# Performance work log

Measured on AMD Instinct MI355X. Metric: run time of the kernel, lower is better.

## Reference

```python
import jax, jax.numpy as jnp
import numpy as np

B, T, D = 1, 2048, 4096
N, K, H = 32, 8, 128  # num_heads, num_kv_heads, head_dim
ROPE_BASE = 10000
SCALE_FACTOR = 1.0
EPS = 1e-6
NEG_INF = -1e9


def rms_norm(x):
    var = jnp.mean(jnp.square(x), axis=-1, keepdims=True)
    return x * jax.lax.rsqrt(var + EPS)


def apply_rope(x, positions, base_frequency, scale_factor=1.0):
    # x: [B, L, num_heads, H], positions: [B, L]
    head_dim = x.shape[-1]
    fraction = 2.0 * jnp.arange(head_dim // 2, dtype=jnp.float32) / head_dim
    timescale = base_frequency ** fraction  # [H/2]
    sinusoid = positions[..., None].astype(jnp.float32) / timescale  # [B,L,H/2]
    sinusoid = sinusoid[..., None, :] / scale_factor  # [B,L,1,H/2]
    sin, cos = jnp.sin(sinusoid), jnp.cos(sinusoid)
    x1, x2 = jnp.split(x, 2, axis=-1)
    return jnp.concatenate([x1 * cos - x2 * sin, x2 * cos + x1 * sin], axis=-1)


def setup_inputs() -> dict:
    key = jax.random.key(0)
    ks = jax.random.split(key, 7)
    x = jax.random.normal(ks[0], (B, T, D), dtype=jnp.float32)
    segment_pos = jnp.broadcast_to(jnp.arange(T, dtype=jnp.int32)[None, :], (B, T))
    causal = jnp.tril(jnp.ones((T, T), dtype=bool))
    attn_mask = jnp.where(causal, 0.0, NEG_INF).astype(jnp.float32)[None]  # [B,T,S]
    attn_mask = jnp.broadcast_to(attn_mask, (B, T, T))
    q_w = jax.random.normal(ks[1], (N, D, H), dtype=jnp.float32) * (D ** -0.5)
    kv_w = jax.random.normal(ks[2], (2, K, D, H), dtype=jnp.float32) * (D ** -0.5)
    o_w = jax.random.normal(ks[3], (N, H, D), dtype=jnp.float32) * ((N * H) ** -0.5)
    q_scale = jax.random.normal(ks[4], (H,), dtype=jnp.float32) * 0.02  # RMSNorm scale (zeros-init style)
    k_scale = jax.random.normal(ks[5], (H,), dtype=jnp.float32) * 0.02
    return {"x": x, "segment_pos": segment_pos, "attn_mask": attn_mask,
            "q_w": q_w, "kv_w": kv_w, "o_w": o_w,
            "q_scale": q_scale, "k_scale": k_scale}


def reference(x, segment_pos, attn_mask, q_w, kv_w, o_w, q_scale, k_scale):
    # Projections
    q = jnp.einsum('BTD,NDH->BTNH', x, q_w)          # [B,T,N,H]
    kv = jnp.einsum('BSD,CKDH->CBSKH', x, kv_w)      # [2,B,S,K,H]
    k, v = kv[0], kv[1]
    # QK RMSNorm (with scale, (1+scale) convention) and value RMSNorm (no scale)
    q = rms_norm(q) * (1.0 + q_scale)
    k = rms_norm(k) * (1.0 + k_scale)
    v = rms_norm(v)
    # RoPE (standard path: positions are [B,L])
    q = apply_rope(q, segment_pos, ROPE_BASE, SCALE_FACTOR)
    k = apply_rope(k, segment_pos, ROPE_BASE, SCALE_FACTOR)
    # GQA grouping: [B,T,K,G,H]
    G = N // K
    qg = q.reshape(B, T, K, G, H)
    attn_logits = jnp.einsum('btkgh,bskh->bkgts', qg, k)  # [B,K,G,T,S]
    attn_logits = attn_logits + attn_mask[:, None, None, :, :]
    attn_weights = jax.nn.softmax(attn_logits, axis=-1).astype(v.dtype)
    out = jnp.einsum('bkgts,bskh->btkgh', attn_weights, v)  # [B,T,K,G,H]
    out = out.reshape(B, T, N, H)
    return jnp.einsum('BTNH,NHD->BTD', out, o_w)
```

## Files before the change

### kernel.cpp

```cpp
#include <hip/hip_runtime.h>
#include <stdint.h>


typedef __bf16 bf16x8 __attribute__((ext_vector_type(8)));
typedef float  f32x4  __attribute__((ext_vector_type(4)));

__device__ __forceinline__ uint16_t f2bf(float f) {
    union { float f; uint32_t u; } v; v.f = f;
    uint32_t r = v.u + 0x7fffu + ((v.u >> 16) & 1u);
    return (uint16_t)(r >> 16);
}

__device__ __forceinline__ void gload_lds16(const void* g, void* l) {
    __builtin_amdgcn_global_load_lds(
        (const __attribute__((address_space(1))) uint32_t*)g,
        (__attribute__((address_space(3))) uint32_t*)l, 16, 0, 0);
}

__global__ __launch_bounds__(256) void k_cvt_x(const float* __restrict__ x,
                                               uint16_t* __restrict__ xb) {
    int i = (blockIdx.x * 256 + threadIdx.x) * 8;
    int r = i >> 12, k = i & 4095;
    float4 a = *(const float4*)(x + i);
    float4 b = *(const float4*)(x + i + 4);
    uint16_t tmp[8];
    tmp[0] = f2bf(a.x); tmp[1] = f2bf(a.y); tmp[2] = f2bf(a.z); tmp[3] = f2bf(a.w);
    tmp[4] = f2bf(b.x); tmp[5] = f2bf(b.y); tmp[6] = f2bf(b.z); tmp[7] = f2bf(b.w);
    int dst = r * 4096 + (k & ~63) + (((((k >> 3) & 7) ^ (r & 7))) << 3);
    *(uint4*)(xb + dst) = *(uint4*)tmp;
}

__global__ __launch_bounds__(256) void k_prep_wt(const float* __restrict__ qw,
                                                 const float* __restrict__ kvw,
                                                 uint16_t* __restrict__ Wt) {
    const int hx = blockIdx.x, dx = blockIdx.y, m = blockIdx.z;
    const float* src = (m < 32) ? (qw + (size_t)m * 524288)
                                : (kvw + (size_t)(m - 32) * 524288);
    __shared__ uint16_t tile[64][65];
    const int t = threadIdx.x, d0 = dx * 64, h0 = hx * 64;
#pragma unroll
    for (int i = 0; i < 16; ++i) {
        int idx = i * 256 + t, r = idx >> 6, c = idx & 63;
        tile[r][c] = f2bf(src[(size_t)(d0 + r) * 128 + h0 + c]);
    }
    __syncthreads();
#pragma unroll
    for (int it = 0; it < 2; ++it) {
        int slot = it * 256 + t, hr = slot >> 3, cl = slot & 7;
        int R = m * 128 + h0 + hr;
        uint16_t tmp[8];
#pragma unroll
        for (int e = 0; e < 8; ++e) tmp[e] = tile[cl * 8 + e][hr];
        *(uint4*)&Wt[(size_t)R * 4096 + d0 + ((cl ^ (R & 7)) << 3)] = *(uint4*)tmp;
    }
}

__global__ __launch_bounds__(256) void k_prep_ot(const float* __restrict__ ow,
                                                 uint16_t* __restrict__ Ot) {
    const int dx = blockIdx.x, hx = blockIdx.y, n = blockIdx.z;
    const float* src = ow + (size_t)n * 524288;
    __shared__ uint16_t tile[64][65];
    const int t = threadIdx.x, h0 = hx * 64, d0 = dx * 64;
#pragma unroll
    for (int i = 0; i < 16; ++i) {
        int idx = i * 256 + t, r = idx >> 6, c = idx & 63;
        tile[r][c] = f2bf(src[(size_t)(h0 + r) * 4096 + d0 + c]);
    }
    __syncthreads();
#pragma unroll
    for (int it = 0; it < 2; ++it) {
        int slot = it * 256 + t, dr = slot >> 3, cl = slot & 7;
        int R = d0 + dr;
        uint16_t tmp[8];
#pragma unroll
        for (int e = 0; e < 8; ++e) tmp[e] = tile[cl * 8 + e][dr];
        *(uint4*)&Ot[(size_t)R * 4096 + n * 128 + h0 + ((cl ^ (R & 7)) << 3)] = *(uint4*)tmp;
    }
}

#define PH_BAR do { asm volatile("" ::: "memory"); \
                    __builtin_amdgcn_s_barrier(); \
                    asm volatile("" ::: "memory"); } while (0)
#define WAIT_VM(N) do { asm volatile("s_waitcnt vmcnt(" #N ")" ::: "memory"); \
                        __builtin_amdgcn_sched_barrier(0); } while (0)
#define SCHED0 __builtin_amdgcn_sched_barrier(0)

__global__ __launch_bounds__(512, 2) void k_gemm_qkv(const uint16_t* __restrict__ A,
                                                     const uint16_t* __restrict__ Bt,
                                                     const int* __restrict__ pos,
                                                     const float* __restrict__ qs,
                                                     const float* __restrict__ ks,
                                                     uint16_t* __restrict__ Qg,
                                                     uint16_t* __restrict__ Kg,
                                                     uint16_t* __restrict__ Vg) {
    extern __shared__ __align__(16) char smem[];
    uint16_t* lds = (uint16_t*)smem;
    const int Kd = 4096;
    const int t = threadIdx.x, wid = t >> 6, lane = t & 63;
    const int l16 = lane & 15, quad = lane >> 4;
    const int wr = wid >> 2, wc = wid & 3;
    const int bx = blockIdx.x, bm0 = blockIdx.y * 256, bn0 = bx * 256;

    f32x4 acc[8][4];
    const f32x4 z4 = {0.f, 0.f, 0.f, 0.f};
#pragma unroll
    for (int i = 0; i < 8; ++i)
#pragma unroll
        for (int j = 0; j < 4; ++j) acc[i][j] = z4;

    const int r0 = wid * 16 + (lane >> 2), c4 = lane & 3;
    const int sw2 = (r0 >> 1) & 3, sw7 = r0 & 7;
    const int offK0 = (((c4 ^ sw2)) ^ sw7) * 8;
    const int offK1 = ((4 + (c4 ^ sw2)) ^ sw7) * 8;
    const uint16_t* pA0 = A + (size_t)(bm0 + r0) * Kd;
    const uint16_t* pA1 = pA0 + (size_t)128 * Kd;
    const uint16_t* pB0 = Bt + (size_t)(bn0 + r0) * Kd;
    const uint16_t* pB1 = pB0 + (size_t)128 * Kd;
    uint16_t* stA = lds + wid * 512;
    uint16_t* stB = lds + 32768 + wid * 512;

    const int sA = (l16 >> 1) & 3;
    const int rdA = (wr * 128 + l16) * 32 + ((quad ^ sA) << 3);
    const int rdB = 32768 + (wc * 64 + l16) * 32 + ((quad ^ sA) << 3);

    bf16x8 afA[4], afB[4], bfA[4], bfB[4];

#define STAGE_A(SLAB, OFF, TT) do { \
    gload_lds16(pA0 + (size_t)(TT) * 64 + (OFF), stA + (SLAB) * 8192); \
    gload_lds16(pA1 + (size_t)(TT) * 64 + (OFF), stA + (SLAB) * 8192 + 4096); } while (0)
#define STAGE_B(SLAB, OFF, TT) do { \
    gload_lds16(pB0 + (size_t)(TT) * 64 + (OFF), stB + (SLAB) * 8192); \
    gload_lds16(pB1 + (size_t)(TT) * 64 + (OFF), stB + (SLAB) * 8192 + 4096); } while (0)
#define RD_A(DST, SLAB, I0) do { _Pragma("unroll") \
    for (int i_ = 0; i_ < 4; ++i_) \
        DST[i_] = *(const bf16x8*)&lds[(SLAB) * 8192 + rdA + ((I0) + i_) * 512]; } while (0)
#define RD_B(DST, SLAB) do { _Pragma("unroll") \
    for (int j_ = 0; j_ < 4; ++j_) \
        DST[j_] = *(const bf16x8*)&lds[(SLAB) * 8192 + rdB + j_ * 512]; } while (0)
#define MFMA16(AF, BF, I0) do { __builtin_amdgcn_s_setprio(1); \
    _Pragma("unroll") for (int i_ = 0; i_ < 4; ++i_) \
        _Pragma("unroll") for (int j_ = 0; j_ < 4; ++j_) \
            acc[(I0) + i_][j_] = __builtin_amdgcn_mfma_f32_16x16x32_bf16(AF[i_], BF[j_], acc[(I0) + i_][j_], 0, 0, 0); \
    __builtin_amdgcn_s_setprio(0); } while (0)

#define TILE(TT, BUF) do { \
    RD_A(afB, 2*(BUF), 4); \
    WAIT_VM(4); \
    STAGE_A(2*((BUF)^1)+1, offK1, (TT)+1); \
    SCHED0; MFMA16(afA, bfA, 0); PH_BAR; \
    RD_A(afA, 2*(BUF)+1, 0); RD_B(bfB, 2*(BUF)+1); \
    STAGE_B(2*((BUF)^1)+1, offK1, (TT)+1); \
    SCHED0; MFMA16(afB, bfA, 4); PH_BAR; \
    RD_A(afB, 2*(BUF)+1, 4); \
    WAIT_VM(4); \
    STAGE_A(2*(BUF), offK0, (TT)+2); \
    SCHED0; MFMA16(afA, bfB, 0); PH_BAR; \
    RD_A(afA, 2*((BUF)^1), 0); RD_B(bfA, 2*((BUF)^1)); \
    STAGE_B(2*(BUF), offK0, (TT)+2); \
    SCHED0; MFMA16(afB, bfB, 4); PH_BAR; \
} while (0)

    STAGE_A(0, offK0, 0); STAGE_B(0, offK0, 0);
    STAGE_A(1, offK1, 0); STAGE_B(1, offK1, 0);
    STAGE_A(2, offK0, 1); STAGE_B(2, offK0, 1);
    WAIT_VM(8);
    PH_BAR;
    RD_A(afA, 0, 0); RD_B(bfA, 0);

#pragma unroll 1
    for (int Ti = 0; Ti < 31; ++Ti) {
        TILE(2 * Ti, 0);
        TILE(2 * Ti + 1, 1);
    }

    RD_A(afB, 0, 4); WAIT_VM(4); STAGE_A(3, offK1, 63);
    SCHED0; MFMA16(afA, bfA, 0); PH_BAR;
    RD_A(afA, 1, 0); RD_B(bfB, 1); STAGE_B(3, offK1, 63);
    SCHED0; MFMA16(afB, bfA, 4); PH_BAR;
    RD_A(afB, 1, 4); WAIT_VM(4);
    SCHED0; MFMA16(afA, bfB, 0); PH_BAR;
    RD_A(afA, 2, 0); RD_B(bfA, 2);
    SCHED0; MFMA16(afB, bfB, 4); PH_BAR;
    RD_A(afB, 2, 4); WAIT_VM(0);
    SCHED0; MFMA16(afA, bfA, 0); PH_BAR;
    RD_A(afA, 3, 0); RD_B(bfB, 3);
    SCHED0; MFMA16(afB, bfA, 4); PH_BAR;
    RD_A(afB, 3, 4);
    SCHED0; MFMA16(afA, bfB, 0); PH_BAR;
    SCHED0; MFMA16(afB, bfB, 4);

#undef TILE
#undef MFMA16
#undef RD_B
#undef RD_A
#undef STAGE_B
#undef STAGE_A

    float* X   = (float*)smem;
    float* ssq = (float*)(smem + 133120);

#pragma unroll
    for (int i = 0; i < 8; ++i)
#pragma unroll
        for (int r = 0; r < 4; ++r) {
            float s = 0.f;
#pragma unroll
            for (int j = 0; j < 4; ++j) s += acc[i][j][r] * acc[i][j][r];
            s += __shfl_xor(s, 1); s += __shfl_xor(s, 2);
            s += __shfl_xor(s, 4); s += __shfl_xor(s, 8);
            if (l16 == 0)
                ssq[(wr * 128 + i * 16 + quad * 4 + r) * 4 + (wc >> 1) * 2 + (wc & 1)] = s;
        }
    __syncthreads();

    const int cat = (bx < 16) ? 0 : (bx < 20 ? 1 : 2);
    float s1 = 0.f, s2 = 0.f, invts = 0.f;
    if (cat < 2) {
        const float* sc = cat ? ks : qs;
        s1 = 1.0f + sc[lane];
        s2 = 1.0f + sc[lane + 64];
        invts = exp2f((float)lane * -0.20762050593046014f);
    }

#pragma unroll
    for (int pass = 0; pass < 2; ++pass) {
        if (wr == pass) {
#pragma unroll
            for (int i = 0; i < 8; ++i)
#pragma unroll
                for (int j = 0; j < 4; ++j)
#pragma unroll
                    for (int r = 0; r < 4; ++r)
                        X[(i * 16 + quad * 4 + r) * 260 + wc * 64 + j * 16 + l16] = acc[i][j][r];
        }
        __syncthreads();
        for (int rr = 0; rr < 16; ++rr) {
            const int lrow = wid * 16 + rr;
            const int grow = bm0 + pass * 128 + lrow;
            float sn = 0.f, cs = 0.f;
            if (cat < 2) {
                float ang = (float)pos[grow] * invts;
                __sincosf(ang, &sn, &cs);
            }
#pragma unroll
            for (int hh = 0; hh < 2; ++hh) {
                const int sb = (pass * 128 + lrow) * 4 + hh * 2;
                float rn = rsqrtf((ssq[sb] + ssq[sb + 1]) * 0.0078125f + 1e-6f);
                float x1 = X[lrow * 260 + hh * 128 + lane];
                float x2 = X[lrow * 260 + hh * 128 + 64 + lane];
                if (cat < 2) {
                    float y1 = x1 * rn * s1, y2 = x2 * rn * s2;
                    X[lrow * 260 + hh * 128 + lane]      = y1 * cs - y2 * sn;
                    X[lrow * 260 + hh * 128 + 64 + lane] = y2 * cs + y1 * sn;
                } else {
                    X[lrow * 260 + hh * 128 + lane]      = x1 * rn;
                    X[lrow * 260 + hh * 128 + 64 + lane] = x2 * rn;
                }
            }
        }
        __syncthreads();
        if (cat == 2) {
#pragma unroll
            for (int it = 0; it < 8; ++it) {
                int slot = it * 512 + t, hh = slot >> 11, rem = slot & 2047;
                int h = rem >> 4, sc2 = rem & 15;
                uint16_t tmp[8];
#pragma unroll
                for (int e = 0; e < 8; ++e)
                    tmp[e] = f2bf(X[(sc2 * 8 + e) * 260 + hh * 128 + h]);
                int n = bx * 2 + hh;
                *(uint4*)&Vg[((size_t)(n - 40) * 128 + h) * 2048 + (bm0 + pass * 128)
                             + ((sc2 ^ (h & 15)) << 3)] = *(uint4*)tmp;
            }
        } else {
#pragma unroll
            for (int it = 0; it < 8; ++it) {
                int slot = it * 512 + t, hh = slot >> 11, rem = slot & 2047;
                int lrow = rem >> 4, c = rem & 15;
                int tg = bm0 + pass * 128 + lrow, n = bx * 2 + hh;
                f32x4 a = *(f32x4*)&X[lrow * 260 + hh * 128 + c * 8];
                f32x4 b = *(f32x4*)&X[lrow * 260 + hh * 128 + c * 8 + 4];
                uint16_t tmp[8];
#pragma unroll
                for (int e = 0; e < 4; ++e) { tmp[e] = f2bf(a[e]); tmp[4 + e] = f2bf(b[e]); }
                if (cat == 0)
                    *(uint4*)&Qg[((size_t)n * 2048 + tg) * 128 + c * 8] = *(uint4*)tmp;
                else
                    *(uint4*)&Kg[((size_t)(n - 32) * 2048 + tg) * 128
                                 + ((c ^ (tg & 15)) << 3)] = *(uint4*)tmp;
            }
        }
        __syncthreads();
    }
}

__global__ __launch_bounds__(512, 2) void k_gemm2p(const uint16_t* __restrict__ A,
                                                   const uint16_t* __restrict__ Bt,
                                                   float* __restrict__ C) {
    extern __shared__ __align__(16) char smem2[];
    uint16_t* lds = (uint16_t*)smem2;
    const int Kd = 4096, Nn = 4096;
    const int t = threadIdx.x, wid = t >> 6, lane = t & 63;
    const int l16 = lane & 15, quad = lane >> 4;
    const int wr = wid >> 1, wc = wid & 1;
    const int bm0 = blockIdx.y * 256, bn0 = blockIdx.x * 128;

    f32x4 acc[4][4];
    const f32x4 z4 = {0.f, 0.f, 0.f, 0.f};
#pragma unroll
    for (int i = 0; i < 4; ++i)
#pragma unroll
        for (int j = 0; j < 4; ++j) acc[i][j] = z4;

    const int r0 = wid * 16 + (lane >> 2), c4 = lane & 3;
    const int sw2 = (r0 >> 1) & 3, sw7 = r0 & 7;
    const int offK0 = ((c4 ^ sw2) ^ sw7) * 8;
    const int offK1 = ((4 + (c4 ^ sw2)) ^ sw7) * 8;
    const uint16_t* pA0 = A + (size_t)(bm0 + r0) * Kd;
    const uint16_t* pA1 = pA0 + (size_t)128 * Kd;
    const uint16_t* pB0 = Bt + (size_t)(bn0 + r0) * Kd;
    uint16_t* stA = lds + wid * 512;
    uint16_t* stB = lds + 49152 + wid * 512;

    const int sA = (l16 >> 1) & 3;
    const int rdA = (wr * 64 + l16) * 32 + ((quad ^ sA) << 3);
    const int rdB = 49152 + (wc * 64 + l16) * 32 + ((quad ^ sA) << 3);

    bf16x8 afA[4], afB[4], bfA[4], bfB[4];

#define G2_STAGE(SLAB, OFF, TT) do { \
    gload_lds16(pA0 + (size_t)(TT) * 64 + (OFF), stA + (SLAB) * 8192); \
    gload_lds16(pA1 + (size_t)(TT) * 64 + (OFF), stA + (SLAB) * 8192 + 4096); \
    gload_lds16(pB0 + (size_t)(TT) * 64 + (OFF), stB + (SLAB) * 4096); } while (0)
#define G2_RD(AD, BD, CS) do { _Pragma("unroll") \
    for (int i_ = 0; i_ < 4; ++i_) \
        AD[i_] = *(const bf16x8*)&lds[(CS) * 8192 + rdA + i_ * 512]; \
    _Pragma("unroll") for (int j_ = 0; j_ < 4; ++j_) \
        BD[j_] = *(const bf16x8*)&lds[(CS) * 4096 + rdB + j_ * 512]; } while (0)
#define G2_MFMA(AF, BF) do { __builtin_amdgcn_s_setprio(1); \
    _Pragma("unroll") for (int i_ = 0; i_ < 4; ++i_) \
        _Pragma("unroll") for (int j_ = 0; j_ < 4; ++j_) \
            acc[i_][j_] = __builtin_amdgcn_mfma_f32_16x16x32_bf16(AF[i_], BF[j_], acc[i_][j_], 0, 0, 0); \
    __builtin_amdgcn_s_setprio(0); } while (0)

#define G2_PH(RA, RB, CSN, SST, OFF, TT, MA, MB) do { \
    G2_RD(RA, RB, CSN); \
    WAIT_VM(3); \
    G2_STAGE(SST, OFF, TT); \
    SCHED0; G2_MFMA(MA, MB); PH_BAR; } while (0)

    G2_STAGE(0, offK0, 0);
    G2_STAGE(1, offK1, 0);
    G2_STAGE(2, offK0, 1);
    G2_STAGE(3, offK1, 1);
    WAIT_VM(6);
    PH_BAR;
    G2_RD(afA, bfA, 0);

#pragma unroll 1
    for (int m = 0; m < 20; ++m) {
        G2_PH(afB, bfB, 1, 4, offK0, 3*m + 2, afA, bfA);
        G2_PH(afA, bfA, 2, 5, offK1, 3*m + 2, afB, bfB);
        G2_PH(afB, bfB, 3, 0, offK0, 3*m + 3, afA, bfA);
        G2_PH(afA, bfA, 4, 1, offK1, 3*m + 3, afB, bfB);
        G2_PH(afB, bfB, 5, 2, offK0, 3*m + 4, afA, bfA);
        G2_PH(afA, bfA, 0, 3, offK1, 3*m + 4, afB, bfB);
    }
    G2_PH(afB, bfB, 1, 4, offK0, 62, afA, bfA);
    G2_PH(afA, bfA, 2, 5, offK1, 62, afB, bfB);
    G2_PH(afB, bfB, 3, 0, offK0, 63, afA, bfA);
    G2_PH(afA, bfA, 4, 1, offK1, 63, afB, bfB);
    G2_RD(afB, bfB, 5); WAIT_VM(3); SCHED0; G2_MFMA(afA, bfA); PH_BAR;
    G2_RD(afA, bfA, 0); WAIT_VM(0); SCHED0; G2_MFMA(afB, bfB); PH_BAR;
    G2_RD(afB, bfB, 1);              SCHED0; G2_MFMA(afA, bfA); PH_BAR;
    SCHED0; G2_MFMA(afB, bfB);

#undef G2_PH
#undef G2_MFMA
#undef G2_RD
#undef G2_STAGE

#pragma unroll
    for (int i = 0; i < 4; ++i)
#pragma unroll
        for (int j = 0; j < 4; ++j) {
            int row = bm0 + wr * 64 + i * 16 + quad * 4;
            int col = bn0 + wc * 64 + j * 16 + l16;
            float* cp = C + (size_t)row * Nn + col;
            cp[0]              = acc[i][j][0];
            cp[(size_t)Nn]     = acc[i][j][1];
            cp[2 * (size_t)Nn] = acc[i][j][2];
            cp[3 * (size_t)Nn] = acc[i][j][3];
        }
}

__global__ __launch_bounds__(512, 2) void k_attn(const uint16_t* __restrict__ Q,
                                                 const uint16_t* __restrict__ K,
                                                 const uint16_t* __restrict__ Vt,
                                                 uint16_t* __restrict__ att) {
    extern __shared__ __align__(16) char asmem[];
    uint16_t* sK = (uint16_t*)asmem;
    uint16_t* sV = sK + 16384;
    uint16_t* sP = sK + 32768;
    const int p = blockIdx.x, n = blockIdx.y, kk = n >> 2;
    const int t = threadIdx.x, wid = t >> 6, lane = t & 63;
    const int l16 = lane & 15, quad = lane >> 4;
    const int grp = wid >> 2, wsub = wid & 3;
    const int nk_a = p + 1, nk_b = 16 - p;
    const int nk_w = grp ? nk_b : nk_a;
    const int qbase = (grp ? (15 - p) * 128 : p * 128) + wsub * 32;
    const f32x4 z4 = {0.f, 0.f, 0.f, 0.f};

    const uint16_t* Kbase = K  + ((size_t)kk * 2048 + wid * 16 + (lane >> 4)) * 128 + (lane & 15) * 8;
    const uint16_t* Vbase = Vt + ((size_t)kk * 128  + wid * 16 + (lane >> 4)) * 2048 + (lane & 15) * 8;
    uint16_t* sPw = sP + wid * 32 * 128;

    bf16x8 qf0[4], qf1[4];
#pragma unroll
    for (int kc = 0; kc < 4; ++kc) {
        qf0[kc] = *(const bf16x8*)(Q + (size_t)(n * 2048 + qbase + l16) * 128 + kc * 32 + quad * 8);
        qf1[kc] = *(const bf16x8*)(Q + (size_t)(n * 2048 + qbase + 16 + l16) * 128 + kc * 32 + quad * 8);
    }

    f32x4 O0[8], O1[8];
#pragma unroll
    for (int h = 0; h < 8; ++h) { O0[h] = z4; O1[h] = z4; }
    float mrow0[4], lrow0[4], mrow1[4], lrow1[4];
#pragma unroll
    for (int r = 0; r < 4; ++r) {
        mrow0[r] = -INFINITY; lrow0[r] = 0.f;
        mrow1[r] = -INFINITY; lrow1[r] = 0.f;
    }

#define SM_SET(S, MR, LR, OO, ROWB, MASKED, S0V) do { \
    if (MASKED) { \
        _Pragma("unroll") for (int jn_ = 0; jn_ < 8; ++jn_) { \
            int sc_ = (S0V) + jn_ * 16 + l16; \
            _Pragma("unroll") for (int r_ = 0; r_ < 4; ++r_) { \
                int mr_ = (ROWB) + quad * 4 + r_; \
                if (sc_ > mr_) S[jn_][r_] = -INFINITY; \
            } \
        } \
    } \
    float alpha_[4]; \
    _Pragma("unroll") for (int r_ = 0; r_ < 4; ++r_) { \
        float mx_ = S[0][r_]; \
        _Pragma("unroll") for (int jn_ = 1; jn_ < 8; ++jn_) mx_ = fmaxf(mx_, S[jn_][r_]); \
        mx_ = fmaxf(mx_, __shfl_xor(mx_, 1)); \
        mx_ = fmaxf(mx_, __shfl_xor(mx_, 2)); \
        mx_ = fmaxf(mx_, __shfl_xor(mx_, 4)); \
        mx_ = fmaxf(mx_, __shfl_xor(mx_, 8)); \
        float mn_ = fmaxf(MR[r_], mx_); \
        float a_ = __expf(MR[r_] - mn_); \
        MR[r_] = mn_; \
        float sum_ = 0.f; \
        _Pragma("unroll") for (int jn_ = 0; jn_ < 8; ++jn_) { \
            float e_ = __expf(S[jn_][r_] - mn_); \
            S[jn_][r_] = e_; \
            sum_ += e_; \
        } \
        sum_ += __shfl_xor(sum_, 1); \
        sum_ += __shfl_xor(sum_, 2); \
        sum_ += __shfl_xor(sum_, 4); \
        sum_ += __shfl_xor(sum_, 8); \
        LR[r_] = LR[r_] * a_ + sum_; \
        alpha_[r_] = a_; \
    } \
    _Pragma("unroll") for (int h_ = 0; h_ < 8; ++h_) \
        _Pragma("unroll") for (int r_ = 0; r_ < 4; ++r_) OO[h_][r_] *= alpha_[r_]; \
} while (0)

    for (int st = 0; st < nk_b; ++st) {
        const int s0 = st * 128;
        __syncthreads();
#pragma unroll
        for (int j = 0; j < 4; ++j) {
            gload_lds16(Kbase + (size_t)(s0 + j * 4) * 128, &sK[(wid * 16 + j * 4) * 128]);
            gload_lds16(Vbase + (size_t)(j * 4) * 2048 + s0, &sV[(wid * 16 + j * 4) * 128]);
        }
        __syncthreads();

        if (st < nk_w) {
            f32x4 S0[8], S1[8];
#pragma unroll
            for (int jn = 0; jn < 8; ++jn) { S0[jn] = z4; S1[jn] = z4; }
#pragma unroll
            for (int jn = 0; jn < 8; ++jn) {
                int krow = jn * 16 + l16;
#pragma unroll
                for (int kc = 0; kc < 4; ++kc) {
                    bf16x8 b = *(const bf16x8*)&sK[krow * 128 + (((kc * 4 + quad) ^ l16) << 3)];
                    S0[jn] = __builtin_amdgcn_mfma_f32_16x16x32_bf16(qf0[kc], b, S0[jn], 0, 0, 0);
                    S1[jn] = __builtin_amdgcn_mfma_f32_16x16x32_bf16(qf1[kc], b, S1[jn], 0, 0, 0);
                }
            }
            const int masked = (st == nk_w - 1);
            SM_SET(S0, mrow0, lrow0, O0, qbase, masked, s0);
            SM_SET(S1, mrow1, lrow1, O1, qbase + 16, masked, s0);

#pragma unroll
            for (int jn = 0; jn < 8; ++jn)
#pragma unroll
                for (int r = 0; r < 4; ++r) {
                    int prow = quad * 4 + r;
                    int pcol = jn * 16 + l16;
                    int off = (pcol & 7) | ((((pcol >> 3) ^ prow) & 15) << 3);
                    sPw[prow * 128 + off]        = f2bf(S0[jn][r]);
                    sPw[(16 + prow) * 128 + off] = f2bf(S1[jn][r]);
                }
            bf16x8 pf0[4], pf1[4];
#pragma unroll
            for (int ksv = 0; ksv < 4; ++ksv) {
                pf0[ksv] = *(const bf16x8*)&sPw[l16 * 128 + (((ksv * 4 + quad) ^ l16) << 3)];
                pf1[ksv] = *(const bf16x8*)&sPw[(16 + l16) * 128 + (((ksv * 4 + quad) ^ l16) << 3)];
            }
#pragma unroll
            for (int hj = 0; hj < 8; ++hj) {
                int vrow = hj * 16 + l16;
#pragma unroll
                for (int ksv = 0; ksv < 4; ++ksv) {
                    bf16x8 b = *(const bf16x8*)&sV[vrow * 128 + (((ksv * 4 + quad) ^ l16) << 3)];
                    O0[hj] = __builtin_amdgcn_mfma_f32_16x16x32_bf16(pf0[ksv], b, O0[hj], 0, 0, 0);
                    O1[hj] = __builtin_amdgcn_mfma_f32_16x16x32_bf16(pf1[ksv], b, O1[hj], 0, 0, 0);
                }
            }
        }
    }
#undef SM_SET

#pragma unroll
    for (int set = 0; set < 2; ++set) {
        float inv[4];
#pragma unroll
        for (int r = 0; r < 4; ++r)
            inv[r] = 1.0f / (set ? lrow1[r] : lrow0[r]);
#pragma unroll
        for (int hj = 0; hj < 8; ++hj)
#pragma unroll
            for (int r = 0; r < 4; ++r) {
                float v = (set ? O1[hj][r] : O0[hj][r]) * inv[r];
                sPw[(quad * 4 + r) * 132 + hj * 16 + l16] = f2bf(v);
            }
#pragma unroll
        for (int it = 0; it < 4; ++it) {
            int slot = it * 64 + lane, rloc = slot >> 4, cl = slot & 15;
            bf16x8 v = *(const bf16x8*)&sPw[rloc * 132 + cl * 8];
            int R = qbase + set * 16 + rloc;
            size_t dst = (size_t)R * 4096 + n * 128 + ((cl & 8) << 3) + (((cl & 7) ^ (R & 7)) << 3);
            *(uint4*)&att[dst] = *(uint4*)&v;
        }
    }
}

extern "C" void kernel_launch(void* const* d_in, const int* in_sizes, int n_in,
                              void* d_out, int out_size, void* d_ws, size_t ws_size,
                              hipStream_t stream) {
    const float* x   = (const float*)d_in[0];
    const int*   sp  = (const int*)d_in[1];
    const float* qw  = (const float*)d_in[3];
    const float* kvw = (const float*)d_in[4];
    const float* ow  = (const float*)d_in[5];
    const float* qsc = (const float*)d_in[6];
    const float* ksc = (const float*)d_in[7];
    float* out = (float*)d_out;

    char* ws = (char*)d_ws;
    uint16_t* xb   = (uint16_t*)(ws);
    uint16_t* Wt   = (uint16_t*)(ws + (size_t)(16u << 20));
    uint16_t* Qb   = (uint16_t*)(ws + (size_t)(64u << 20));
    uint16_t* Kb   = (uint16_t*)(ws + (size_t)(80u << 20));
    uint16_t* Vtb  = (uint16_t*)(ws + (size_t)(84u << 20));
    uint16_t* att  = (uint16_t*)(ws);
    uint16_t* Ot   = (uint16_t*)(ws + (size_t)(16u << 20));

    static bool attr_done = false;
    if (!attr_done) {
        hipFuncSetAttribute(reinterpret_cast<const void*>(k_gemm_qkv),
                            hipFuncAttributeMaxDynamicSharedMemorySize, 137216);
        hipFuncSetAttribute(reinterpret_cast<const void*>(k_gemm2p),
                            hipFuncAttributeMaxDynamicSharedMemorySize, 147456);
        hipFuncSetAttribute(reinterpret_cast<const void*>(k_attn),
                            hipFuncAttributeMaxDynamicSharedMemorySize, 131072);
        attr_done = true;
    }

    k_cvt_x    <<<4096, 256, 0, stream>>>(x, xb);
    k_prep_wt  <<<dim3(2, 64, 48), 256, 0, stream>>>(qw, kvw, Wt);
    k_gemm_qkv <<<dim3(24, 8), 512, 137216, stream>>>(xb, Wt, sp, qsc, ksc, Qb, Kb, Vtb);
    k_prep_ot  <<<dim3(64, 2, 32), 256, 0, stream>>>(ow, Ot);
    k_attn     <<<dim3(8, 32), 512, 131072, stream>>>(Qb, Kb, Vtb, att);
    k_gemm2p   <<<dim3(32, 8), 512, 147456, stream>>>(att, Ot, out);
}
```

Baseline: 521.9 us.

## Merge prep kernels, fold O-weight transpose into QKV GEMM, retile output GEMM

Merges the x conversion and QKV weight transpose into one launch. When the workspace is large enough, extra blocks are added to the QKV GEMM grid that transpose the output-projection weights, so that work overlaps with the GEMM tail and one launch is removed. The output GEMM is rewritten as a 256-thread 128x128-tile kernel with a 4-slab pipeline and less LDS, giving more blocks and more occupancy. The risks are a tail imbalance from the extra blocks and a different pipelining schedule in the output GEMM.

```diff
diff --git a/kernel.cpp b/kernel.cpp
--- a/kernel.cpp
+++ b/kernel.cpp
@@ -17,27 +17,30 @@
         (__attribute__((address_space(3))) uint32_t*)l, 16, 0, 0);
 }
 
-__global__ __launch_bounds__(256) void k_cvt_x(const float* __restrict__ x,
-                                               uint16_t* __restrict__ xb) {
-    int i = (blockIdx.x * 256 + threadIdx.x) * 8;
-    int r = i >> 12, k = i & 4095;
-    float4 a = *(const float4*)(x + i);
-    float4 b = *(const float4*)(x + i + 4);
-    uint16_t tmp[8];
-    tmp[0] = f2bf(a.x); tmp[1] = f2bf(a.y); tmp[2] = f2bf(a.z); tmp[3] = f2bf(a.w);
-    tmp[4] = f2bf(b.x); tmp[5] = f2bf(b.y); tmp[6] = f2bf(b.z); tmp[7] = f2bf(b.w);
-    int dst = r * 4096 + (k & ~63) + (((((k >> 3) & 7) ^ (r & 7))) << 3);
-    *(uint4*)(xb + dst) = *(uint4*)tmp;
-}
-
-__global__ __launch_bounds__(256) void k_prep_wt(const float* __restrict__ qw,
-                                                 const float* __restrict__ kvw,
-                                                 uint16_t* __restrict__ Wt) {
-    const int hx = blockIdx.x, dx = blockIdx.y, m = blockIdx.z;
+__global__ __launch_bounds__(256) void k_prep(const float* __restrict__ x,
+                                              uint16_t* __restrict__ xb,
+                                              const float* __restrict__ qw,
+                                              const float* __restrict__ kvw,
+                                              uint16_t* __restrict__ Wt) {
+    __shared__ uint16_t tile[64][65];
+    const int b = blockIdx.x, t = threadIdx.x;
+    if (b < 4096) {
+        int i = (b * 256 + t) * 8;
+        int r = i >> 12, k = i & 4095;
+        float4 a = *(const float4*)(x + i);
+        float4 c = *(const float4*)(x + i + 4);
+        uint16_t tmp[8];
+        tmp[0] = f2bf(a.x); tmp[1] = f2bf(a.y); tmp[2] = f2bf(a.z); tmp[3] = f2bf(a.w);
+        tmp[4] = f2bf(c.x); tmp[5] = f2bf(c.y); tmp[6] = f2bf(c.z); tmp[7] = f2bf(c.w);
+        int dst = r * 4096 + (k & ~63) + (((((k >> 3) & 7) ^ (r & 7))) << 3);
+        *(uint4*)(xb + dst) = *(uint4*)tmp;
+        return;
+    }
+    const int bid = b - 4096;
+    const int m = bid >> 7, rem = bid & 127, dx = rem >> 1, hx = rem & 1;
     const float* src = (m < 32) ? (qw + (size_t)m * 524288)
                                 : (kvw + (size_t)(m - 32) * 524288);
-    __shared__ uint16_t tile[64][65];
-    const int t = threadIdx.x, d0 = dx * 64, h0 = hx * 64;
+    const int d0 = dx * 64, h0 = hx * 64;
 #pragma unroll
     for (int i = 0; i < 16; ++i) {
         int idx = i * 256 + t, r = idx >> 6, c = idx & 63;
@@ -83,6 +86,8 @@
                     asm volatile("" ::: "memory"); } while (0)
 #define WAIT_VM(N) do { asm volatile("s_waitcnt vmcnt(" #N ")" ::: "memory"); \
                         __builtin_amdgcn_sched_barrier(0); } while (0)
+#define WAIT_LGKM do { asm volatile("s_waitcnt lgkmcnt(0)" ::: "memory"); \
+                       __builtin_amdgcn_sched_barrier(0); } while (0)
 #define SCHED0 __builtin_amdgcn_sched_barrier(0)
 
 __global__ __launch_bounds__(512, 2) void k_gemm_qkv(const uint16_t* __restrict__ A,
@@ -92,14 +97,49 @@
                                                      const float* __restrict__ ks,
                                                      uint16_t* __restrict__ Qg,
                                                      uint16_t* __restrict__ Kg,
-                                                     uint16_t* __restrict__ Vg) {
+                                                     uint16_t* __restrict__ Vg,
+                                                     const float* __restrict__ ow,
+                                                     uint16_t* __restrict__ Ot) {
     extern __shared__ __align__(16) char smem[];
+    const int t = threadIdx.x;
+    const int bx = blockIdx.x;
+
+    if (bx >= 24) {
+        uint16_t* tl = (uint16_t*)smem + (t >> 8) * 64 * 65;
+        const int tt = t & 255;
+        const int jb = ((bx - 24) * 8 + blockIdx.y) * 64;
+        for (int it = 0; it < 32; ++it) {
+            int job = jb + it * 2 + (t >> 8);
+            int n2 = job & 31, hx = (job >> 5) & 1, dx = job >> 6;
+            const float* src = ow + (size_t)n2 * 524288;
+            const int h0 = hx * 64, d0 = dx * 64;
+#pragma unroll
+            for (int i = 0; i < 16; ++i) {
+                int idx = i * 256 + tt, r = idx >> 6, c = idx & 63;
+                tl[r * 65 + c] = f2bf(src[(size_t)(h0 + r) * 4096 + d0 + c]);
+            }
+            __syncthreads();
+#pragma unroll
+            for (int it2 = 0; it2 < 2; ++it2) {
+                int slot = it2 * 256 + tt, dr = slot >> 3, cl = slot & 7;
+                int R = d0 + dr;
+                uint16_t tmp[8];
+#pragma unroll
+                for (int e = 0; e < 8; ++e) tmp[e] = tl[(cl * 8 + e) * 65 + dr];
+                *(uint4*)&Ot[(size_t)R * 4096 + n2 * 128 + h0 + ((cl ^ (R & 7)) << 3)]
+                    = *(uint4*)tmp;
+            }
+            __syncthreads();
+        }
+        return;
+    }
+
     uint16_t* lds = (uint16_t*)smem;
     const int Kd = 4096;
-    const int t = threadIdx.x, wid = t >> 6, lane = t & 63;
+    const int wid = t >> 6, lane = t & 63;
     const int l16 = lane & 15, quad = lane >> 4;
     const int wr = wid >> 2, wc = wid & 3;
-    const int bx = blockIdx.x, bm0 = blockIdx.y * 256, bn0 = bx * 256;
+    const int bm0 = blockIdx.y * 256, bn0 = bx * 256;
 
     f32x4 acc[8][4];
     const f32x4 z4 = {0.f, 0.f, 0.f, 0.f};
@@ -294,7 +334,7 @@
     }
 }
 
-__global__ __launch_bounds__(512, 2) void k_gemm2p(const uint16_t* __restrict__ A,
+__global__ __launch_bounds__(256, 2) void k_gemm2b(const uint16_t* __restrict__ A,
                                                    const uint16_t* __restrict__ Bt,
                                                    float* __restrict__ C) {
     extern __shared__ __align__(16) char smem2[];
@@ -303,7 +343,7 @@
     const int t = threadIdx.x, wid = t >> 6, lane = t & 63;
     const int l16 = lane & 15, quad = lane >> 4;
     const int wr = wid >> 1, wc = wid & 1;
-    const int bm0 = blockIdx.y * 256, bn0 = blockIdx.x * 128;
+    const int bm0 = blockIdx.y * 128, bn0 = blockIdx.x * 128;
 
     f32x4 acc[4][4];
     const f32x4 z4 = {0.f, 0.f, 0.f, 0.f};
@@ -312,73 +352,67 @@
 #pragma unroll
         for (int j = 0; j < 4; ++j) acc[i][j] = z4;
 
-    const int r0 = wid * 16 + (lane >> 2), c4 = lane & 3;
+    const int r0 = wid * 32 + (lane >> 2), c4 = lane & 3;
     const int sw2 = (r0 >> 1) & 3, sw7 = r0 & 7;
     const int offK0 = ((c4 ^ sw2) ^ sw7) * 8;
     const int offK1 = ((4 + (c4 ^ sw2)) ^ sw7) * 8;
     const uint16_t* pA0 = A + (size_t)(bm0 + r0) * Kd;
-    const uint16_t* pA1 = pA0 + (size_t)128 * Kd;
+    const uint16_t* pA1 = pA0 + (size_t)16 * Kd;
     const uint16_t* pB0 = Bt + (size_t)(bn0 + r0) * Kd;
-    uint16_t* stA = lds + wid * 512;
-    uint16_t* stB = lds + 49152 + wid * 512;
+    const uint16_t* pB1 = pB0 + (size_t)16 * Kd;
+    uint16_t* stA = lds + wid * 1024;
+    uint16_t* stB = lds + 16384 + wid * 1024;
 
     const int sA = (l16 >> 1) & 3;
     const int rdA = (wr * 64 + l16) * 32 + ((quad ^ sA) << 3);
-    const int rdB = 49152 + (wc * 64 + l16) * 32 + ((quad ^ sA) << 3);
-
-    bf16x8 afA[4], afB[4], bfA[4], bfB[4];
-
-#define G2_STAGE(SLAB, OFF, TT) do { \
-    gload_lds16(pA0 + (size_t)(TT) * 64 + (OFF), stA + (SLAB) * 8192); \
-    gload_lds16(pA1 + (size_t)(TT) * 64 + (OFF), stA + (SLAB) * 8192 + 4096); \
-    gload_lds16(pB0 + (size_t)(TT) * 64 + (OFF), stB + (SLAB) * 4096); } while (0)
-#define G2_RD(AD, BD, CS) do { _Pragma("unroll") \
+    const int rdB = (wc * 64 + l16) * 32 + ((quad ^ sA) << 3);
+
+    bf16x8 af[4], bf[4];
+
+#define B2_STAGE(SLAB, OFF, TT) do { \
+    gload_lds16(pA0 + (size_t)(TT) * 64 + (OFF), stA + (SLAB) * 4096); \
+    gload_lds16(pA1 + (size_t)(TT) * 64 + (OFF), stA + (SLAB) * 4096 + 512); \
+    gload_lds16(pB0 + (size_t)(TT) * 64 + (OFF), stB + (SLAB) * 4096); \
+    gload_lds16(pB1 + (size_t)(TT) * 64 + (OFF), stB + (SLAB) * 4096 + 512); } while (0)
+#define B2_RD(CS) do { _Pragma("unroll") \
     for (int i_ = 0; i_ < 4; ++i_) \
-        AD[i_] = *(const bf16x8*)&lds[(CS) * 8192 + rdA + i_ * 512]; \
+        af[i_] = *(const bf16x8*)&lds[(CS) * 4096 + rdA + i_ * 512]; \
     _Pragma("unroll") for (int j_ = 0; j_ < 4; ++j_) \
-        BD[j_] = *(const bf16x8*)&lds[(CS) * 4096 + rdB + j_ * 512]; } while (0)
-#define G2_MFMA(AF, BF) do { __builtin_amdgcn_s_setprio(1); \
+        bf[j_] = *(const bf16x8*)&lds[16384 + (CS) * 4096 + rdB + j_ * 512]; } while (0)
+#define B2_MFMA do { __builtin_amdgcn_s_setprio(1); \
     _Pragma("unroll") for (int i_ = 0; i_ < 4; ++i_) \
         _Pragma("unroll") for (int j_ = 0; j_ < 4; ++j_) \
-            acc[i_][j_] = __builtin_amdgcn_mfma_f32_16x16x32_bf16(AF[i_], BF[j_], acc[i_][j_], 0, 0, 0); \
+            acc[i_][j_] = __builtin_amdgcn_mfma_f32_16x16x32_bf16(af[i_], bf[j_], acc[i_][j_], 0, 0, 0); \
     __builtin_amdgcn_s_setprio(0); } while (0)
-
-#define G2_PH(RA, RB, CSN, SST, OFF, TT, MA, MB) do { \
-    G2_RD(RA, RB, CSN); \
-    WAIT_VM(3); \
-    G2_STAGE(SST, OFF, TT); \
-    SCHED0; G2_MFMA(MA, MB); PH_BAR; } while (0)
-
-    G2_STAGE(0, offK0, 0);
-    G2_STAGE(1, offK1, 0);
-    G2_STAGE(2, offK0, 1);
-    G2_STAGE(3, offK1, 1);
-    WAIT_VM(6);
+#define B2_PH(CS, SG, OFF, TT) do { \
+    B2_RD(CS); \
+    B2_STAGE(SG, OFF, TT); \
+    WAIT_VM(8); \
+    PH_BAR; WAIT_LGKM; \
+    B2_MFMA; PH_BAR; } while (0)
+
+    B2_STAGE(0, offK0, 0);
+    B2_STAGE(1, offK1, 0);
+    B2_STAGE(2, offK0, 1);
+    WAIT_VM(8);
     PH_BAR;
-    G2_RD(afA, bfA, 0);
 
 #pragma unroll 1
-    for (int m = 0; m < 20; ++m) {
-        G2_PH(afB, bfB, 1, 4, offK0, 3*m + 2, afA, bfA);
-        G2_PH(afA, bfA, 2, 5, offK1, 3*m + 2, afB, bfB);
-        G2_PH(afB, bfB, 3, 0, offK0, 3*m + 3, afA, bfA);
-        G2_PH(afA, bfA, 4, 1, offK1, 3*m + 3, afB, bfB);
-        G2_PH(afB, bfB, 5, 2, offK0, 3*m + 4, afA, bfA);
-        G2_PH(afA, bfA, 0, 3, offK1, 3*m + 4, afB, bfB);
-    }
-    G2_PH(afB, bfB, 1, 4, offK0, 62, afA, bfA);
-    G2_PH(afA, bfA, 2, 5, offK1, 62, afB, bfB);
-    G2_PH(afB, bfB, 3, 0, offK0, 63, afA, bfA);
-    G2_PH(afA, bfA, 4, 1, offK1, 63, afB, bfB);
-    G2_RD(afB, bfB, 5); WAIT_VM(3); SCHED0; G2_MFMA(afA, bfA); PH_BAR;
-    G2_RD(afA, bfA, 0); WAIT_VM(0); SCHED0; G2_MFMA(afB, bfB); PH_BAR;
-    G2_RD(afB, bfB, 1);              SCHED0; G2_MFMA(afA, bfA); PH_BAR;
-    SCHED0; G2_MFMA(afB, bfB);
-
-#undef G2_PH
-#undef G2_MFMA
-#undef G2_RD
-#undef G2_STAGE
+    for (int m = 0; m < 31; ++m) {
+        B2_PH(0, 3, offK1, 2 * m + 1);
+        B2_PH(1, 0, offK0, 2 * m + 2);
+        B2_PH(2, 1, offK1, 2 * m + 2);
+        B2_PH(3, 2, offK0, 2 * m + 3);
+    }
+    B2_PH(0, 3, offK1, 63);
+    B2_RD(1); WAIT_VM(4); PH_BAR; WAIT_LGKM; B2_MFMA; PH_BAR;
+    B2_RD(2); WAIT_VM(0); PH_BAR; WAIT_LGKM; B2_MFMA; PH_BAR;
+    B2_RD(3);             PH_BAR; WAIT_LGKM; B2_MFMA;
+
+#undef B2_PH
+#undef B2_MFMA
+#undef B2_RD
+#undef B2_STAGE
 
 #pragma unroll
     for (int i = 0; i < 4; ++i)
@@ -406,8 +440,8 @@
     const int t = threadIdx.x, wid = t >> 6, lane = t & 63;
     const int l16 = lane & 15, quad = lane >> 4;
     const int grp = wid >> 2, wsub = wid & 3;
-    const int nk_a = p + 1, nk_b = 16 - p;
-    const int nk_w = grp ? nk_b : nk_a;
+    const int nk_b = 16 - p;
+    const int nk_w = grp ? nk_b : (p + 1);
     const int qbase = (grp ? (15 - p) * 128 : p * 128) + wsub * 32;
     const f32x4 z4 = {0.f, 0.f, 0.f, 0.f};
 
@@ -571,23 +605,30 @@
     uint16_t* Kb   = (uint16_t*)(ws + (size_t)(80u << 20));
     uint16_t* Vtb  = (uint16_t*)(ws + (size_t)(84u << 20));
     uint16_t* att  = (uint16_t*)(ws);
-    uint16_t* Ot   = (uint16_t*)(ws + (size_t)(16u << 20));
+
+    const bool fused = ws_size >= ((size_t)120u << 20);
+    uint16_t* Ot = (uint16_t*)(ws + ((size_t)(fused ? 88u : 16u) << 20));
 
     static bool attr_done = false;
     if (!attr_done) {
         hipFuncSetAttribute(reinterpret_cast<const void*>(k_gemm_qkv),
                             hipFuncAttributeMaxDynamicSharedMemorySize, 137216);
-        hipFuncSetAttribute(reinterpret_cast<const void*>(k_gemm2p),
-                            hipFuncAttributeMaxDynamicSharedMemorySize, 147456);
+        hipFuncSetAttribute(reinterpret_cast<const void*>(k_gemm2b),
+                            hipFuncAttributeMaxDynamicSharedMemorySize, 65536);
         hipFuncSetAttribute(reinterpret_cast<const void*>(k_attn),
                             hipFuncAttributeMaxDynamicSharedMemorySize, 131072);
         attr_done = true;
     }
 
-    k_cvt_x    <<<4096, 256, 0, stream>>>(x, xb);
-    k_prep_wt  <<<dim3(2, 64, 48), 256, 0, stream>>>(qw, kvw, Wt);
-    k_gemm_qkv <<<dim3(24, 8), 512, 137216, stream>>>(xb, Wt, sp, qsc, ksc, Qb, Kb, Vtb);
-    k_prep_ot  <<<dim3(64, 2, 32), 256, 0, stream>>>(ow, Ot);
-    k_attn     <<<dim3(8, 32), 512, 131072, stream>>>(Qb, Kb, Vtb, att);
-    k_gemm2p   <<<dim3(32, 8), 512, 147456, stream>>>(att, Ot, out);
-}
+    k_prep <<<10240, 256, 0, stream>>>(x, xb, qw, kvw, Wt);
+    if (fused) {
+        k_gemm_qkv <<<dim3(32, 8), 512, 137216, stream>>>(xb, Wt, sp, qsc, ksc,
+                                                          Qb, Kb, Vtb, ow, Ot);
+    } else {
+        k_gemm_qkv <<<dim3(24, 8), 512, 137216, stream>>>(xb, Wt, sp, qsc, ksc,
+                                                          Qb, Kb, Vtb, ow, Ot);
+        k_prep_ot  <<<dim3(64, 2, 32), 256, 0, stream>>>(ow, Ot);
+    }
+    k_attn   <<<dim3(8, 32), 512, 131072, stream>>>(Qb, Kb, Vtb, att);
+    k_gemm2b <<<dim3(32, 16), 256, 65536, stream>>>(att, Ot, out);
+}
```

Result: faster. 509.6 us (-2.4%).
